# Performance work log

Hardware: AMD Instinct MI355X
Metric: run time of the kernel (lower is better)

## Reference

```python
import jax, jax.numpy as jnp
import numpy as np

B, S, H = 8, 4096, 512

def setup_inputs() -> dict:
    key = jax.random.key(0)
    k1, k2 = jax.random.split(key)
    lstm_out = jax.random.normal(k1, (B, S, H), dtype=jnp.float32)
    W = jax.random.normal(k2, (2 * H, H), dtype=jnp.float32) * (1.0 / np.sqrt(H))
    b = jnp.zeros((2 * H,), dtype=jnp.float32)
    return {"lstm_out": lstm_out, "W": W, "b": b}

def reference(lstm_out, W, b):
    # noise_net: Linear(H, 2H) + Softplus
    noise = jax.nn.softplus(jnp.einsum('bsh,oh->bso', lstm_out, W) + b)  # [B,S,2H]
    Q = noise[:, :, :H]   # process noise
    R = noise[:, :, H:]   # observation noise

    def step(carry, inp):
        state, P = carry
        z, q, r = inp                      # each [B,H]
        P_pred = P + q
        K = P_pred / (P_pred + r + 1e-6)
        state = state + K * (z - state)
        P = (1.0 - K) * P_pred
        return (state, P), state

    state0 = lstm_out[:, 0, :]
    P0 = jnp.full_like(state0, 0.1)
    # time-major for scan: [S,B,H]
    xs = (jnp.swapaxes(lstm_out, 0, 1),
          jnp.swapaxes(Q, 0, 1),
          jnp.swapaxes(R, 0, 1))
    _, states = jax.lax.scan(step, (state0, P0), xs)  # [S,B,H]
    return jnp.swapaxes(states, 0, 1)  # [B,S,H]
```

## Files before the change

kernel.cpp:

```cpp
#include <hip/hip_runtime.h>
#include <hip/hip_bf16.h>

#define B_ 8
#define S_ 4096
#define H_ 512

using short8 = __attribute__((ext_vector_type(8))) short;
using f32x4  = __attribute__((ext_vector_type(4))) float;

__device__ __forceinline__ float bf2f(unsigned u16) {
    return __uint_as_float(u16 << 16);
}
__device__ __forceinline__ unsigned pk2bf(float x, float y) {
    __hip_bfloat162 h = __float22bfloat162_rn(make_float2(x, y));
    return *reinterpret_cast<unsigned*>(&h);
}
__device__ __forceinline__ float softplus_f(float x) {
    float sp = __logf(1.0f + __expf(x));
    return x > 15.0f ? x : sp;
}

typedef __attribute__((address_space(1))) void* gbl_ptr_t;
typedef __attribute__((address_space(3))) void* lds_ptr_t;
__device__ __forceinline__ void gload_lds16(const void* g, void* l) {
    __builtin_amdgcn_global_load_lds((gbl_ptr_t)g, (lds_ptr_t)l, 16, 0, 0);
}

#define BAR() do { asm volatile("" ::: "memory"); \
                   __builtin_amdgcn_s_barrier(); \
                   asm volatile("" ::: "memory"); } while (0)

#define ASZ4 4194304u
#define TOT4 4325376u

__global__ __launch_bounds__(256)
void convert_bf16(const float* __restrict__ A, const float* __restrict__ Wm,
                  uint2* __restrict__ dst) {
    for (unsigned i = blockIdx.x * 256u + threadIdx.x; i < TOT4; i += 2048u * 256u) {
        const float4* p = (i < ASZ4) ? ((const float4*)A) + i
                                     : ((const float4*)Wm) + (i - ASZ4);
        const float4 v = *p;
        uint2 o;
        o.x = pk2bf(v.x, v.y);
        o.y = pk2bf(v.z, v.w);
        dst[i] = o;
    }
}

#define TM 256
#define TN 256
#define BK 32

__global__ __launch_bounds__(512, 2)
void gemm_softplus(const unsigned short* __restrict__ Ab,
                   const unsigned short* __restrict__ Wb,
                   const float* __restrict__ bias,
                   unsigned* __restrict__ QR) {
    __shared__ unsigned short As[2][8192];
    __shared__ unsigned short Bs[2][8192];

    const int bid     = blockIdx.x;
    const int logical = (bid & 7) * 64 + (bid >> 3);
    const int bm = logical >> 2;
    const int bn = logical & 3;

    const int t      = threadIdx.x;
    const int wave   = t >> 6;
    const int lane   = t & 63;
    const int wave_m = wave >> 2;
    const int wave_n = wave & 3;
    const int wm  = wave_m * 128;
    const int wn  = wave_n * 64;
    const int l15 = lane & 15;
    const int l4  = lane >> 4;

    const int m0 = bm * TM;

    const int lr2  = lane >> 2;
    const int s_st = (lr2 + (lane >> 4)) & 3;
    const int sg   = ((lane & 3) ^ s_st) * 8;
    const int row0 = wave * 16 + lr2;
    const int nr0 = bn * 128 + ((row0 >> 6) << 5) + (row0 & 31) + (((row0 >> 5) & 1) << 9);
    const unsigned short* agA0 = Ab + (size_t)(m0 + row0) * 512 + sg;
    const unsigned short* agA1 = agA0 + (size_t)128 * 512;
    const unsigned short* bgB0 = Wb + (size_t)nr0 * 512 + sg;
    const unsigned short* bgB1 = bgB0 + (size_t)64 * 512;
    const int sd = wave * 512;

    const int s_rd = (l15 + (l15 >> 2)) & 3;
    const int gsw  = (l4 ^ s_rd) * 8;
    const int aoff = (wm + l15) * 32 + gsw;
    const int boff = (wn + l15) * 32 + gsw;

    f32x4 acc[8][4] = {};

#define STAGE(s) do { \
    const int _sl = (s) & 1; const int _kc = (s) * BK; \
    gload_lds16(agA0 + _kc, &As[_sl][sd]); \
    gload_lds16(agA1 + _kc, &As[_sl][sd + 4096]); \
    gload_lds16(bgB0 + _kc, &Bs[_sl][sd]); \
    gload_lds16(bgB1 + _kc, &Bs[_sl][sd + 4096]); \
} while (0)

#define SLICE(g, VMN, DOSTG) do { \
    const unsigned short* _a = &As[(g) & 1][0]; \
    const unsigned short* _b = &Bs[(g) & 1][0]; \
    if (DOSTG) STAGE((g) + 1); \
    asm volatile("s_waitcnt vmcnt(" #VMN ")" ::: "memory"); \
    BAR(); \
    short8 af[8], bf[4]; \
    _Pragma("unroll") for (int j = 0; j < 4; ++j) \
        bf[j] = *(const short8*)(_b + boff + j * 512); \
    _Pragma("unroll") for (int i = 0; i < 8; ++i) \
        af[i] = *(const short8*)(_a + aoff + i * 512); \
    __builtin_amdgcn_s_setprio(1); \
    _Pragma("unroll") for (int i = 0; i < 8; ++i) \
    _Pragma("unroll") for (int j = 0; j < 4; ++j) \
        acc[i][j] = __builtin_amdgcn_mfma_f32_16x16x32_bf16(af[i], bf[j], acc[i][j], 0, 0, 0); \
    __builtin_amdgcn_s_setprio(0); \
    BAR(); \
} while (0)

    STAGE(0);
    for (int g = 0; g < 15; ++g) {
        SLICE(g, 4, 1);
    }
    SLICE(15, 0, 0);

#undef SLICE
#undef STAGE

#pragma unroll
    for (int j = 0; j < 2; ++j) {
        const int h  = bn * 128 + (wn >> 1) + j * 16 + l15;
        const float bq = bias[h];
        const float br = bias[h + 512];
#pragma unroll
        for (int i = 0; i < 8; ++i) {
            const int mb = m0 + wm + i * 16 + l4 * 4;
#pragma unroll
            for (int r = 0; r < 4; ++r) {
                const float qv = softplus_f(acc[i][j][r] + bq);
                const float rv = softplus_f(acc[i][j + 2][r] + br);
                QR[(size_t)(mb + r) * 512 + h] = pk2bf(qv, rv);
            }
        }
    }
}

#define CHUNK 128
#define WARM 64

__global__ __launch_bounds__(256, 2)
void kalman_scan(const float* __restrict__ z,
                 const unsigned* __restrict__ QR,
                 float* __restrict__ out) {
    const int t     = threadIdx.x;
    const int hb    = blockIdx.x & 1;
    const int b     = (blockIdx.x >> 1) & 7;
    const int chunk = blockIdx.x >> 4;
    const int h     = hb * 256 + t;
    const int s0    = chunk << 7;
    const int sw    = (chunk == 0) ? 0 : (s0 - WARM);
    const size_t base = ((size_t)(b * S_ + sw)) * 512 + h;

    const float*    zp  = z + base;
    const unsigned* qrp = (const unsigned*)QR + base;
    float*          op  = out + base;

    const int ng    = ((s0 + CHUNK) - sw) >> 3;
    const int skipg = (s0 - sw) >> 3;

    float    Z0[8], Z1[8], Z2[8], Z3[8], Z4[8], Z5[8], Z6[8], Z7[8];
    unsigned Q0[8], Q1[8], Q2[8], Q3[8], Q4[8], Q5[8], Q6[8], Q7[8];

#define LOADG(g, Zb, Qb) { const int _o = (g) * 8;                          \
    _Pragma("unroll") for (int u = 0; u < 8; ++u) {                         \
        Zb[u] = zp[(size_t)(_o + u) * 512]; Qb[u] = qrp[(size_t)(_o + u) * 512]; } }

#define COMP(g, Zb, Qb) { const int _o = (g) * 8; const bool _st = (g) >= skipg; \
    _Pragma("unroll") for (int u = 0; u < 8; ++u) {                         \
        const float q  = bf2f(Qb[u] & 0xffffu);                             \
        const float r  = bf2f(Qb[u] >> 16);                                 \
        const float Pp = P + q, rr = r + 1e-6f;                             \
        const float K  = Pp * __builtin_amdgcn_rcpf(Pp + rr);               \
        state = fmaf(K, Zb[u] - state, state); P = rr * K;                  \
        if (_st) op[(size_t)(_o + u) * 512] = state; } }

    LOADG(0, Z0, Q0); LOADG(1, Z1, Q1); LOADG(2, Z2, Q2); LOADG(3, Z3, Q3);

    float state = Z0[0];
    float P = 0.1f;

    for (int g = 0; g < ng; g += 8) {
        if (g + 4  < ng) LOADG(g + 4,  Z4, Q4); COMP(g,     Z0, Q0);
        if (g + 5  < ng) LOADG(g + 5,  Z5, Q5); COMP(g + 1, Z1, Q1);
        if (g + 6  < ng) LOADG(g + 6,  Z6, Q6); COMP(g + 2, Z2, Q2);
        if (g + 7  < ng) LOADG(g + 7,  Z7, Q7); COMP(g + 3, Z3, Q3);
        if (g + 8  < ng) LOADG(g + 8,  Z0, Q0); COMP(g + 4, Z4, Q4);
        if (g + 9  < ng) LOADG(g + 9,  Z1, Q1); COMP(g + 5, Z5, Q5);
        if (g + 10 < ng) LOADG(g + 10, Z2, Q2); COMP(g + 6, Z6, Q6);
        if (g + 11 < ng) LOADG(g + 11, Z3, Q3); COMP(g + 7, Z7, Q7);
    }
#undef LOADG
#undef COMP
}

extern "C" void kernel_launch(void* const* d_in, const int* in_sizes, int n_in,
                              void* d_out, int out_size, void* d_ws, size_t ws_size,
                              hipStream_t stream) {
    const float* lstm = (const float*)d_in[0];
    const float* Wm   = (const float*)d_in[1];
    const float* bias = (const float*)d_in[2];

    unsigned* QRw = (unsigned*)d_ws;

    unsigned short* Abf = (unsigned short*)d_out;
    unsigned short* Wbf = (unsigned short*)((char*)d_out + (32u << 20));

    hipLaunchKernelGGL(convert_bf16, dim3(2048), dim3(256), 0, stream,
                       lstm, Wm, (uint2*)Abf);

    hipLaunchKernelGGL(gemm_softplus, dim3(512), dim3(512), 0, stream,
                       Abf, Wbf, bias, QRw);

    hipLaunchKernelGGL(kalman_scan, dim3(512), dim3(256), 0, stream,
                       lstm, QRw, (float*)d_out);
}
```

Before: 210.3 us.

## Deepen GEMM K-tile to 64 with dynamic-LDS double buffering and split fragment loads

The bf16 GEMM now stages 64-wide K tiles, each as two 32-wide halves, into a 128 KB dynamic shared-memory double buffer. The loads for the next tile's halves are issued while the current tile's halves are computed. A-fragments are loaded in two groups of four, which lowers register pressure, and the LDS swizzle pattern is adjusted. The aim is fewer barrier round-trips per unit of K and better overlap of global-to-LDS copies with MFMA work. In exchange, the kernel needs 128 KB of LDS per block, which likely limits it to one resident block per CU instead of two.

```diff
diff --git a/kernel.cpp b/kernel.cpp
--- a/kernel.cpp
+++ b/kernel.cpp
@@ -49,15 +49,16 @@
 
 #define TM 256
 #define TN 256
-#define BK 32
+#define KT 64
 
 __global__ __launch_bounds__(512, 2)
 void gemm_softplus(const unsigned short* __restrict__ Ab,
                    const unsigned short* __restrict__ Wb,
                    const float* __restrict__ bias,
                    unsigned* __restrict__ QR) {
-    __shared__ unsigned short As[2][8192];
-    __shared__ unsigned short Bs[2][8192];
+    extern __shared__ __align__(16) unsigned short smem[];
+    unsigned short* Asm = smem;
+    unsigned short* Bsm = smem + 32768;
 
     const int bid     = blockIdx.x;
     const int logical = (bid & 7) * 64 + (bid >> 3);
@@ -76,58 +77,77 @@
 
     const int m0 = bm * TM;
 
-    const int lr2  = lane >> 2;
-    const int s_st = (lr2 + (lane >> 4)) & 3;
-    const int sg   = ((lane & 3) ^ s_st) * 8;
-    const int row0 = wave * 16 + lr2;
+    const int q_  = lane >> 2;
+    const int g_  = lane & 3;
+    const int sgo = (g_ ^ ((q_ >> 1) & 3)) * 8;
+    const int row0 = wave * 16 + q_;
     const int nr0 = bn * 128 + ((row0 >> 6) << 5) + (row0 & 31) + (((row0 >> 5) & 1) << 9);
-    const unsigned short* agA0 = Ab + (size_t)(m0 + row0) * 512 + sg;
+    const unsigned short* agA0 = Ab + (size_t)(m0 + row0) * 512 + sgo;
     const unsigned short* agA1 = agA0 + (size_t)128 * 512;
-    const unsigned short* bgB0 = Wb + (size_t)nr0 * 512 + sg;
+    const unsigned short* bgB0 = Wb + (size_t)nr0 * 512 + sgo;
     const unsigned short* bgB1 = bgB0 + (size_t)64 * 512;
-    const int sd = wave * 512;
-
-    const int s_rd = (l15 + (l15 >> 2)) & 3;
-    const int gsw  = (l4 ^ s_rd) * 8;
+    const int sdw = wave * 512;
+
+    const int gsw  = (l4 ^ ((l15 >> 1) & 3)) * 8;
     const int aoff = (wm + l15) * 32 + gsw;
     const int boff = (wn + l15) * 32 + gsw;
 
     f32x4 acc[8][4] = {};
 
-#define STAGE(s) do { \
-    const int _sl = (s) & 1; const int _kc = (s) * BK; \
-    gload_lds16(agA0 + _kc, &As[_sl][sd]); \
-    gload_lds16(agA1 + _kc, &As[_sl][sd + 4096]); \
-    gload_lds16(bgB0 + _kc, &Bs[_sl][sd]); \
-    gload_lds16(bgB1 + _kc, &Bs[_sl][sd + 4096]); \
+#define STAGE(tt, kh) do { \
+    const int _kc = (tt) * KT + (kh) * 32; \
+    const int _db = ((tt) & 1) * 16384 + (kh) * 8192; \
+    gload_lds16(agA0 + _kc, Asm + _db + sdw); \
+    gload_lds16(agA1 + _kc, Asm + _db + sdw + 4096); \
+    gload_lds16(bgB0 + _kc, Bsm + _db + sdw); \
+    gload_lds16(bgB1 + _kc, Bsm + _db + sdw + 4096); \
 } while (0)
 
-#define SLICE(g, VMN, DOSTG) do { \
-    const unsigned short* _a = &As[(g) & 1][0]; \
-    const unsigned short* _b = &Bs[(g) & 1][0]; \
-    if (DOSTG) STAGE((g) + 1); \
-    asm volatile("s_waitcnt vmcnt(" #VMN ")" ::: "memory"); \
-    BAR(); \
-    short8 af[8], bf[4]; \
-    _Pragma("unroll") for (int j = 0; j < 4; ++j) \
-        bf[j] = *(const short8*)(_b + boff + j * 512); \
-    _Pragma("unroll") for (int i = 0; i < 8; ++i) \
-        af[i] = *(const short8*)(_a + aoff + i * 512); \
+#define MMA16(ibase) do { \
     __builtin_amdgcn_s_setprio(1); \
-    _Pragma("unroll") for (int i = 0; i < 8; ++i) \
-    _Pragma("unroll") for (int j = 0; j < 4; ++j) \
-        acc[i][j] = __builtin_amdgcn_mfma_f32_16x16x32_bf16(af[i], bf[j], acc[i][j], 0, 0, 0); \
+    _Pragma("unroll") for (int ii = 0; ii < 4; ++ii) \
+    _Pragma("unroll") for (int jj = 0; jj < 4; ++jj) \
+        acc[(ibase) + ii][jj] = __builtin_amdgcn_mfma_f32_16x16x32_bf16( \
+            af[ii], bf[jj], acc[(ibase) + ii][jj], 0, 0, 0); \
     __builtin_amdgcn_s_setprio(0); \
-    BAR(); \
 } while (0)
 
-    STAGE(0);
-    for (int g = 0; g < 15; ++g) {
-        SLICE(g, 4, 1);
-    }
-    SLICE(15, 0, 0);
-
-#undef SLICE
+#define TILE(tt, VM0, VM2, DOSTG) do { \
+    const unsigned short* _a = Asm + ((tt) & 1) * 16384; \
+    const unsigned short* _b = Bsm + ((tt) & 1) * 16384; \
+    short8 af[4], bf[4]; \
+    BAR();                                \
+    if (DOSTG) STAGE((tt) + 1, 0); \
+    asm volatile("s_waitcnt vmcnt(" #VM0 ")" ::: "memory"); \
+    BAR();                                \
+    _Pragma("unroll") for (int jj = 0; jj < 4; ++jj) \
+        bf[jj] = *(const short8*)(_b + boff + jj * 512); \
+    _Pragma("unroll") for (int ii = 0; ii < 4; ++ii) \
+        af[ii] = *(const short8*)(_a + aoff + ii * 512); \
+    MMA16(0); \
+    _Pragma("unroll") for (int ii = 0; ii < 4; ++ii) \
+        af[ii] = *(const short8*)(_a + aoff + (ii + 4) * 512); \
+    MMA16(4); \
+    if (DOSTG) STAGE((tt) + 1, 1); \
+    asm volatile("s_waitcnt vmcnt(" #VM2 ")" ::: "memory"); \
+    BAR();                                \
+    _Pragma("unroll") for (int jj = 0; jj < 4; ++jj) \
+        bf[jj] = *(const short8*)(_b + 8192 + boff + jj * 512); \
+    _Pragma("unroll") for (int ii = 0; ii < 4; ++ii) \
+        af[ii] = *(const short8*)(_a + 8192 + aoff + ii * 512); \
+    MMA16(0); \
+    _Pragma("unroll") for (int ii = 0; ii < 4; ++ii) \
+        af[ii] = *(const short8*)(_a + 8192 + aoff + (ii + 4) * 512); \
+    MMA16(4); \
+} while (0)
+
+    STAGE(0, 0); STAGE(0, 1);
+
+    for (int tt = 0; tt < 7; ++tt) TILE(tt, 8, 8, 1);
+    TILE(7, 4, 0, 0);
+
+#undef TILE
+#undef MMA16
 #undef STAGE
 
 #pragma unroll
@@ -218,10 +238,17 @@
     unsigned short* Abf = (unsigned short*)d_out;
     unsigned short* Wbf = (unsigned short*)((char*)d_out + (32u << 20));
 
+    static bool lds_set = false;
+    if (!lds_set) {
+        hipFuncSetAttribute(reinterpret_cast<const void*>(&gemm_softplus),
+                            hipFuncAttributeMaxDynamicSharedMemorySize, 131072);
+        lds_set = true;
+    }
+
     hipLaunchKernelGGL(convert_bf16, dim3(2048), dim3(256), 0, stream,
                        lstm, Wm, (uint2*)Abf);
 
-    hipLaunchKernelGGL(gemm_softplus, dim3(512), dim3(512), 0, stream,
+    hipLaunchKernelGGL(gemm_softplus, dim3(512), dim3(512), 131072, stream,
                        Abf, Wbf, bias, QRw);
 
     hipLaunchKernelGGL(kalman_scan, dim3(512), dim3(256), 0, stream,
```

Measured after the change: 197.8 us. 1.06x faster.
